# Kernel tuning notes

Hardware: AMD Instinct MI355X
Metric: run time of the kernel (lower is better)

Reference implementation:

```python
import jax, jax.numpy as jnp
import numpy as np

N = 512          # input_dim (nodes, fully connected)
T = 16           # time_dim
F = 4            # feature_dim
D = T * F        # node_attr_dim = 64
B = 16           # batch
NEG_SLOPE = 0.2  # GATv2Conv default


def setup_inputs() -> dict:
    key = jax.random.key(0)
    ks = jax.random.split(key, 10)
    s = 0.05
    return {
        "inputs": jax.random.normal(ks[0], (B, N * D), dtype=jnp.float32),
        "Wl": jax.random.normal(ks[1], (D, D), dtype=jnp.float32) * s,  # lin_l weight
        "bl": jax.random.normal(ks[2], (D,), dtype=jnp.float32) * s,
        "Wr": jax.random.normal(ks[3], (D, D), dtype=jnp.float32) * s,  # lin_r weight
        "br": jax.random.normal(ks[4], (D,), dtype=jnp.float32) * s,
        "att": jax.random.normal(ks[5], (D,), dtype=jnp.float32) * s,   # attention vector a
        "bias": jax.random.normal(ks[6], (D,), dtype=jnp.float32) * s,  # GATv2 output bias
        "Wf": jax.random.normal(ks[7], (1, D), dtype=jnp.float32) * s,  # fusion Linear
        "bf": jax.random.normal(ks[8], (1,), dtype=jnp.float32) * s,
    }


def reference(inputs, Wl, bl, Wr, br, att, bias, Wf, bf):
    # GATv2Conv (heads=1) over a fully-connected graph -> dense attention per sample.
    def per_sample(x_flat):
        x = x_flat.reshape(N, D)              # [N, D] node features
        xl = x @ Wl.T + bl                    # source-side transform (lin_l)
        xr = x @ Wr.T + br                    # target-side transform (lin_r)
        # edge (j -> i): e_ij = a . leaky_relu(xl[j] + xr[i])
        s = jax.nn.leaky_relu(xr[:, None, :] + xl[None, :, :], NEG_SLOPE)  # [i, j, d]
        e = jnp.einsum('ijd,d->ij', s, att)   # [N, N] scores
        alpha = jax.nn.softmax(e, axis=-1)    # softmax over sources j per target i
        out = alpha @ xl + bias               # [N, D] aggregated messages
        fused = out @ Wf.T + bf               # [N, 1] fusion linear
        return fused[:, 0]                    # [N]

    return jax.vmap(per_sample)(inputs)       # [B, N]
```

## Files before the change

### kernel.cpp

```cpp
#include <hip/hip_runtime.h>
#include <hip/hip_fp16.h>

#define BB 16
#define NN 512
#define DD 64
#define ROWS (BB * NN)
#define RB 32
#define JCH 32
#define CHUNK (NN / JCH)

typedef _Float16 v8h __attribute__((ext_vector_type(8)));
typedef float    v4f __attribute__((ext_vector_type(4)));

static __device__ __forceinline__ __half2 h2bits(unsigned int u) {
    union { unsigned int i; __half2 h; } c; c.i = u; return c.h;
}
static __device__ __forceinline__ unsigned int bits2(__half2 h) {
    union { __half2 h; unsigned int i; } c; c.h = h; return c.i;
}
static __device__ __forceinline__ __half2 absterm(unsigned int s, unsigned int u,
                                                  unsigned int v, __half2 a) {
    return __hfma2(h2bits(s), __habs2(__hadd2(h2bits(u), h2bits(v))), a);
}
static __device__ __forceinline__ v8h load_cvt8(const float* __restrict__ p) {
    const float4 a = *reinterpret_cast<const float4*>(p);
    const float4 b = *reinterpret_cast<const float4*>(p + 4);
    v8h r;
    r[0] = (_Float16)a.x; r[1] = (_Float16)a.y; r[2] = (_Float16)a.z; r[3] = (_Float16)a.w;
    r[4] = (_Float16)b.x; r[5] = (_Float16)b.y; r[6] = (_Float16)b.z; r[7] = (_Float16)b.w;
    return r;
}

__global__ __launch_bounds__(256, 2) void k1_transform(
    const float* __restrict__ x,
    const float* __restrict__ Wl, const float* __restrict__ bl,
    const float* __restrict__ Wr, const float* __restrict__ br,
    const float* __restrict__ att, const float* __restrict__ bias,
    const float* __restrict__ Wf, const float* __restrict__ bf,
    unsigned int* __restrict__ uh, unsigned int* __restrict__ vh,
    float2* __restrict__ epj,
    unsigned int* __restrict__ sgnh, float* __restrict__ cterm)
{
    __shared__ float xacc[RB][132];
    __shared__ float red[RB][16][2];

    const int tid = threadIdx.x;
    const int r0 = blockIdx.x * RB;

    {
        const int w    = tid >> 6;
        const int lane = tid & 63;
        const int rowhalf = w >> 1;
        const int colhalf = w & 1;
        const int kb = (lane >> 4) * 8;

        const int arow = r0 + rowhalf * 16 + (lane & 15);
        const v8h A0 = load_cvt8(&x[(size_t)arow * DD + 0  + kb]);
        const v8h A1 = load_cvt8(&x[(size_t)arow * DD + 32 + kb]);

        v4f acc[4];
        #pragma unroll
        for (int t = 0; t < 4; ++t) acc[t] = (v4f){0.f, 0.f, 0.f, 0.f};

        #pragma unroll
        for (int t = 0; t < 4; ++t) {
            const int c = colhalf * 64 + t * 16 + (lane & 15);
            const float* wrow = (c < 64) ? (Wl + (size_t)c * DD)
                                         : (Wr + (size_t)(c - 64) * DD);
            const v8h B0 = load_cvt8(wrow + 0  + kb);
            const v8h B1 = load_cvt8(wrow + 32 + kb);
            acc[t] = __builtin_amdgcn_mfma_f32_16x16x32_f16(A0, B0, acc[t], 0, 0, 0);
            acc[t] = __builtin_amdgcn_mfma_f32_16x16x32_f16(A1, B1, acc[t], 0, 0, 0);
        }

        const int rbase = rowhalf * 16 + (lane >> 4) * 4;
        #pragma unroll
        for (int t = 0; t < 4; ++t) {
            const int col = colhalf * 64 + t * 16 + (lane & 15);
            #pragma unroll
            for (int r = 0; r < 4; ++r)
                xacc[rbase + r][col] = acc[t][r];
        }
    }
    __syncthreads();

    {
        const int g  = tid & 31;
        const int rq = tid >> 5;
        const int c0 = g * 4;
        const int ra = rq * 4;
        const bool isL = (c0 < 64);
        const int d0 = c0 & 63;

        const float4 bv = *reinterpret_cast<const float4*>((isL ? bl : br) + d0);
        const float4 av = *reinterpret_cast<const float4*>(&att[d0]);
        const float4 wfv = *reinterpret_cast<const float4*>(&Wf[d0]);

        unsigned int* const dst = isL ? vh : uh;
        const int q    = d0 >> 3;
        const int slot = (d0 & 4) ? 2 : 0;
        const int base = ((r0 >> 9) * 8 + q) * 512 + (r0 & 511);

        #pragma unroll
        for (int r = 0; r < 4; ++r) {
            float4 val = *reinterpret_cast<const float4*>(&xacc[ra + r][c0]);
            val.x += bv.x; val.y += bv.y; val.z += bv.z; val.w += bv.w;

            if (isL) {
                red[ra + r][g][0] = av.x * val.x + av.y * val.y + av.z * val.z + av.w * val.w;
                red[ra + r][g][1] = wfv.x * val.x + wfv.y * val.y + wfv.z * val.z + wfv.w * val.w;
            }
            uint2 pk;
            pk.x = bits2(__floats2half2_rn(0.4f * av.x * val.x, 0.4f * av.y * val.y));
            pk.y = bits2(__floats2half2_rn(0.4f * av.z * val.z, 0.4f * av.w * val.w));
            *reinterpret_cast<uint2*>(&dst[(size_t)(base + ra + r) * 4 + slot]) = pk;
        }
    }
    __syncthreads();

    if (tid < RB) {
        float a = 0.f, p = 0.f;
        #pragma unroll
        for (int gg = 0; gg < 16; ++gg) {
            a += red[tid][gg][0];
            p += red[tid][gg][1];
        }
        const float E = __expf(0.6f * a);
        epj[r0 + tid] = make_float2(E, E * p);
    }

    if (blockIdx.x == 0) {
        if (tid < 32) {
            const float s0 = (att[2 * tid]     >= 0.f) ? 1.f : -1.f;
            const float s1 = (att[2 * tid + 1] >= 0.f) ? 1.f : -1.f;
            sgnh[tid] = bits2(__floats2half2_rn(s0, s1));
        }
        if (tid == 0) {
            float ct = bf[0];
            #pragma unroll 8
            for (int d = 0; d < DD; ++d) ct = fmaf(bias[d], Wf[d], ct);
            *cterm = ct;
        }
    }
}

__global__ __launch_bounds__(512, 2) void k2_attn(
    const unsigned int* __restrict__ uh, const unsigned int* __restrict__ vh,
    const float2* __restrict__ epj, const unsigned int* __restrict__ sgnh,
    float2* __restrict__ part)
{
    const int b  = blockIdx.x >> 5;
    const int jc = blockIdx.x & 31;
    const int i  = threadIdx.x;

    uint4 uu[8];
    #pragma unroll
    for (int q = 0; q < 8; ++q)
        uu[q] = *reinterpret_cast<const uint4*>(&uh[(size_t)(((b * 8 + q) << 9) + i) * 4]);

    uint4 sg[8];
    #pragma unroll
    for (int q = 0; q < 8; ++q)
        sg[q] = reinterpret_cast<const uint4*>(sgnh)[q];

    float s = 0.f, sp = 0.f;
    const int j0 = jc * CHUNK;

    #pragma unroll 2
    for (int jj = 0; jj < CHUNK; ++jj) {
        const int j = j0 + jj;
        __half2 a0 = __float2half2_rn(0.f), a1 = a0;
        #pragma unroll
        for (int q = 0; q < 8; ++q) {
            const uint4 vq = *reinterpret_cast<const uint4*>(
                &vh[(size_t)(((b * 8 + q) << 9) + j) * 4]);
            a0 = absterm(sg[q].x, uu[q].x, vq.x, a0);
            a1 = absterm(sg[q].y, uu[q].y, vq.y, a1);
            a0 = absterm(sg[q].z, uu[q].z, vq.z, a0);
            a1 = absterm(sg[q].w, uu[q].w, vq.w, a1);
        }
        const __half2 h = __hadd2(a0, a1);
        const float f = __low2float(h) + __high2float(h);
        const float t = __expf(f);
        const float2 ep = epj[(b << 9) + j];
        s  = fmaf(t, ep.x, s);
        sp = fmaf(t, ep.y, sp);
    }
    part[(size_t)(((b << 5) + jc) << 9) + i] = make_float2(s, sp);
}

__global__ __launch_bounds__(256) void k3_final(
    const float2* __restrict__ part, const float* __restrict__ cterm,
    float* __restrict__ out)
{
    const int t = blockIdx.x * 256 + threadIdx.x;
    const int b = t >> 9, i = t & 511;
    float s = 0.f, sp = 0.f;
    #pragma unroll
    for (int jc = 0; jc < JCH; ++jc) {
        const float2 v = part[(size_t)(((b << 5) + jc) << 9) + i];
        s  += v.x;
        sp += v.y;
    }
    out[t] = sp / s + *cterm;
}

extern "C" void kernel_launch(void* const* d_in, const int* in_sizes, int n_in,
                              void* d_out, int out_size, void* d_ws, size_t ws_size,
                              hipStream_t stream) {
    const float* x    = (const float*)d_in[0];
    const float* Wl   = (const float*)d_in[1];
    const float* bl   = (const float*)d_in[2];
    const float* Wr   = (const float*)d_in[3];
    const float* br   = (const float*)d_in[4];
    const float* att  = (const float*)d_in[5];
    const float* bias = (const float*)d_in[6];
    const float* Wf   = (const float*)d_in[7];
    const float* bf   = (const float*)d_in[8];
    float* out = (float*)d_out;

    unsigned char* ws = (unsigned char*)d_ws;
    unsigned int* uh   = (unsigned int*)ws;
    unsigned int* vh   = uh + (size_t)ROWS * 32;
    float2*       part = (float2*)(vh + (size_t)ROWS * 32);
    float2*       epj  = part + (size_t)BB * JCH * NN;
    unsigned int* sgnh = (unsigned int*)(epj + ROWS);
    float*        ctp  = (float*)(sgnh + 32);

    k1_transform<<<ROWS / RB, 256, 0, stream>>>(x, Wl, bl, Wr, br, att, bias, Wf, bf,
                                                uh, vh, epj, sgnh, ctp);
    k2_attn<<<BB * JCH, 512, 0, stream>>>(uh, vh, epj, sgnh, part);
    k3_final<<<ROWS / 256, 256, 0, stream>>>(part, ctp, out);
}
```

Before: 28.98 us.

## Stream source rows through scalar loads with double-buffered s_load in attention kernel

The source-side vectors vh are now stored row-contiguous, so k2 can fetch each j row (128 bytes) plus its exp terms with s_load_dwordx16 into SGPRs. Two row buffers are double-buffered, with explicit lgkmcnt waits in inline asm. This replaces per-lane vector loads of wave-uniform data. The j-chunk count doubles to 64 with a higher occupancy bound, and k3 uses smaller blocks. The cost is a larger partials buffer to reduce and fragile hand-written asm synchronisation.

```diff
diff --git a/kernel.cpp b/kernel.cpp
--- a/kernel.cpp
+++ b/kernel.cpp
@@ -6,11 +6,13 @@
 #define DD 64
 #define ROWS (BB * NN)
 #define RB 32
-#define JCH 32
+#define JCH 64
 #define CHUNK (NN / JCH)
 
-typedef _Float16 v8h __attribute__((ext_vector_type(8)));
-typedef float    v4f __attribute__((ext_vector_type(4)));
+typedef _Float16 v8h  __attribute__((ext_vector_type(8)));
+typedef float    v4f  __attribute__((ext_vector_type(4)));
+typedef unsigned int u32x16 __attribute__((ext_vector_type(16)));
+typedef unsigned int u32x2v __attribute__((ext_vector_type(2)));
 
 static __device__ __forceinline__ __half2 h2bits(unsigned int u) {
     union { unsigned int i; __half2 h; } c; c.i = u; return c.h;
@@ -96,24 +98,26 @@
         const float4 av = *reinterpret_cast<const float4*>(&att[d0]);
         const float4 wfv = *reinterpret_cast<const float4*>(&Wf[d0]);
 
-        unsigned int* const dst = isL ? vh : uh;
         const int q    = d0 >> 3;
         const int slot = (d0 & 4) ? 2 : 0;
-        const int base = ((r0 >> 9) * 8 + q) * 512 + (r0 & 511);
+        const int ubase = ((r0 >> 9) * 8 + q) * 512 + (r0 & 511);
 
         #pragma unroll
         for (int r = 0; r < 4; ++r) {
             float4 val = *reinterpret_cast<const float4*>(&xacc[ra + r][c0]);
             val.x += bv.x; val.y += bv.y; val.z += bv.z; val.w += bv.w;
 
+            uint2 pk;
+            pk.x = bits2(__floats2half2_rn(0.4f * av.x * val.x, 0.4f * av.y * val.y));
+            pk.y = bits2(__floats2half2_rn(0.4f * av.z * val.z, 0.4f * av.w * val.w));
+
             if (isL) {
                 red[ra + r][g][0] = av.x * val.x + av.y * val.y + av.z * val.z + av.w * val.w;
                 red[ra + r][g][1] = wfv.x * val.x + wfv.y * val.y + wfv.z * val.z + wfv.w * val.w;
+                *reinterpret_cast<uint2*>(&vh[(size_t)(r0 + ra + r) * 32 + (d0 >> 1)]) = pk;
+            } else {
+                *reinterpret_cast<uint2*>(&uh[(size_t)(ubase + ra + r) * 4 + slot]) = pk;
             }
-            uint2 pk;
-            pk.x = bits2(__floats2half2_rn(0.4f * av.x * val.x, 0.4f * av.y * val.y));
-            pk.y = bits2(__floats2half2_rn(0.4f * av.z * val.z, 0.4f * av.w * val.w));
-            *reinterpret_cast<uint2*>(&dst[(size_t)(base + ra + r) * 4 + slot]) = pk;
         }
     }
     __syncthreads();
@@ -144,13 +148,37 @@
     }
 }
 
-__global__ __launch_bounds__(512, 2) void k2_attn(
+#define SCORE(X0, X1, EP)                                                   \
+    {                                                                       \
+        __half2 a0 = __float2half2_rn(0.f), a1 = a0, a2 = a0, a3 = a0;      \
+        _Pragma("unroll")                                                   \
+        for (int q = 0; q < 4; ++q) {                                       \
+            a0 = absterm(sg[q].x, uu[q].x, X0[q * 4 + 0], a0);              \
+            a1 = absterm(sg[q].y, uu[q].y, X0[q * 4 + 1], a1);              \
+            a2 = absterm(sg[q].z, uu[q].z, X0[q * 4 + 2], a2);              \
+            a3 = absterm(sg[q].w, uu[q].w, X0[q * 4 + 3], a3);              \
+        }                                                                   \
+        _Pragma("unroll")                                                   \
+        for (int q = 0; q < 4; ++q) {                                       \
+            a0 = absterm(sg[q + 4].x, uu[q + 4].x, X1[q * 4 + 0], a0);      \
+            a1 = absterm(sg[q + 4].y, uu[q + 4].y, X1[q * 4 + 1], a1);      \
+            a2 = absterm(sg[q + 4].z, uu[q + 4].z, X1[q * 4 + 2], a2);      \
+            a3 = absterm(sg[q + 4].w, uu[q + 4].w, X1[q * 4 + 3], a3);      \
+        }                                                                   \
+        const __half2 hh = __hadd2(__hadd2(a0, a1), __hadd2(a2, a3));       \
+        const float f = __low2float(hh) + __high2float(hh);                 \
+        const float t = __expf(f);                                          \
+        s  = fmaf(t, __uint_as_float(EP[0]), s);                            \
+        sp = fmaf(t, __uint_as_float(EP[1]), sp);                           \
+    }
+
+__global__ __launch_bounds__(512, 6) void k2_attn(
     const unsigned int* __restrict__ uh, const unsigned int* __restrict__ vh,
     const float2* __restrict__ epj, const unsigned int* __restrict__ sgnh,
     float2* __restrict__ part)
 {
-    const int b  = blockIdx.x >> 5;
-    const int jc = blockIdx.x & 31;
+    const int b  = blockIdx.x >> 6;
+    const int jc = blockIdx.x & 63;
     const int i  = threadIdx.x;
 
     uint4 uu[8];
@@ -163,42 +191,55 @@
     for (int q = 0; q < 8; ++q)
         sg[q] = reinterpret_cast<const uint4*>(sgnh)[q];
 
+    const int j0 = jc * CHUNK;
+    const unsigned int* vrow = vh + (size_t)(b * NN + j0) * 32;
+    const float2* erow = epj + b * NN + j0;
+
+    u32x16 A0, A1, B0, B1;
+    u32x2v eA, eB;
+
+    asm volatile("s_load_dwordx16 %0, %1, 0x0"  : "=s"(A0) : "s"(vrow));
+    asm volatile("s_load_dwordx16 %0, %1, 0x40" : "=s"(A1) : "s"(vrow));
+    asm volatile("s_load_dwordx2  %0, %1, 0x0"  : "=s"(eA) : "s"(erow));
+
     float s = 0.f, sp = 0.f;
-    const int j0 = jc * CHUNK;
-
-    #pragma unroll 2
-    for (int jj = 0; jj < CHUNK; ++jj) {
-        const int j = j0 + jj;
-        __half2 a0 = __float2half2_rn(0.f), a1 = a0;
-        #pragma unroll
-        for (int q = 0; q < 8; ++q) {
-            const uint4 vq = *reinterpret_cast<const uint4*>(
-                &vh[(size_t)(((b * 8 + q) << 9) + j) * 4]);
-            a0 = absterm(sg[q].x, uu[q].x, vq.x, a0);
-            a1 = absterm(sg[q].y, uu[q].y, vq.y, a1);
-            a0 = absterm(sg[q].z, uu[q].z, vq.z, a0);
-            a1 = absterm(sg[q].w, uu[q].w, vq.w, a1);
-        }
-        const __half2 h = __hadd2(a0, a1);
-        const float f = __low2float(h) + __high2float(h);
-        const float t = __expf(f);
-        const float2 ep = epj[(b << 9) + j];
-        s  = fmaf(t, ep.x, s);
-        sp = fmaf(t, ep.y, sp);
-    }
-    part[(size_t)(((b << 5) + jc) << 9) + i] = make_float2(s, sp);
-}
-
-__global__ __launch_bounds__(256) void k3_final(
+
+    #pragma unroll
+    for (int p = 0; p < CHUNK / 2; ++p) {
+        asm volatile("s_waitcnt lgkmcnt(0)" : "+s"(A0), "+s"(A1), "+s"(eA));
+        {
+            const unsigned int* vn = vrow + (2 * p + 1) * 32;
+            const float2* en = erow + (2 * p + 1);
+            asm volatile("s_load_dwordx16 %0, %1, 0x0"  : "=s"(B0) : "s"(vn));
+            asm volatile("s_load_dwordx16 %0, %1, 0x40" : "=s"(B1) : "s"(vn));
+            asm volatile("s_load_dwordx2  %0, %1, 0x0"  : "=s"(eB) : "s"(en));
+        }
+        SCORE(A0, A1, eA);
+
+        asm volatile("s_waitcnt lgkmcnt(0)" : "+s"(B0), "+s"(B1), "+s"(eB));
+        if (p + 1 < CHUNK / 2) {
+            const unsigned int* vn = vrow + (2 * p + 2) * 32;
+            const float2* en = erow + (2 * p + 2);
+            asm volatile("s_load_dwordx16 %0, %1, 0x0"  : "=s"(A0) : "s"(vn));
+            asm volatile("s_load_dwordx16 %0, %1, 0x40" : "=s"(A1) : "s"(vn));
+            asm volatile("s_load_dwordx2  %0, %1, 0x0"  : "=s"(eA) : "s"(en));
+        }
+        SCORE(B0, B1, eB);
+    }
+
+    part[(size_t)(((b << 6) + jc) << 9) + i] = make_float2(s, sp);
+}
+
+__global__ __launch_bounds__(128) void k3_final(
     const float2* __restrict__ part, const float* __restrict__ cterm,
     float* __restrict__ out)
 {
-    const int t = blockIdx.x * 256 + threadIdx.x;
+    const int t = blockIdx.x * 128 + threadIdx.x;
     const int b = t >> 9, i = t & 511;
     float s = 0.f, sp = 0.f;
-    #pragma unroll
+    #pragma unroll 8
     for (int jc = 0; jc < JCH; ++jc) {
-        const float2 v = part[(size_t)(((b << 5) + jc) << 9) + i];
+        const float2 v = part[(size_t)(((b << 6) + jc) << 9) + i];
         s  += v.x;
         sp += v.y;
     }
@@ -230,5 +271,5 @@
     k1_transform<<<ROWS / RB, 256, 0, stream>>>(x, Wl, bl, Wr, br, att, bias, Wf, bf,
                                                 uh, vh, epj, sgnh, ctp);
     k2_attn<<<BB * JCH, 512, 0, stream>>>(uh, vh, epj, sgnh, part);
-    k3_final<<<ROWS / 256, 256, 0, stream>>>(part, ctp, out);
-}
+    k3_final<<<ROWS / 128, 128, 0, stream>>>(part, ctp, out);
+}
```

New measurement: 37.43 us. 1.29x slower.
